# Kernel optimization log

Hardware: AMD Instinct MI355X
Metric: run time of the kernel (lower is better)

Reference implementation:

```python
import jax, jax.numpy as jnp
import numpy as np

N, E, D_IN, D_H, D_OUT = 50000, 800000, 128, 128, 40
EPS = 1e-5


def setup_inputs() -> dict:
    key = jax.random.key(0)
    ks = jax.random.split(key, 12)
    x = jax.random.normal(ks[0], (N, D_IN), dtype=jnp.float32)
    edge_index = jax.random.randint(ks[1], (2, E), 0, N, dtype=jnp.int32)
    s = 1.0 / np.sqrt(D_H)
    return {
        "x": x,
        "edge_index": edge_index,
        "W1": jax.random.normal(ks[2], (D_IN, D_H), jnp.float32) * s,
        "b1": jnp.zeros((D_H,), jnp.float32),
        "W2": jax.random.normal(ks[3], (D_H, D_H), jnp.float32) * s,
        "b2": jnp.zeros((D_H,), jnp.float32),
        "g1": jnp.ones((D_H,), jnp.float32),
        "be1": jnp.zeros((D_H,), jnp.float32),
        "g2": jnp.ones((D_H,), jnp.float32),
        "be2": jnp.zeros((D_H,), jnp.float32),
        "g3": jnp.ones((D_H,), jnp.float32),
        "be3": jnp.zeros((D_H,), jnp.float32),
        "Wm": jax.random.normal(ks[4], (D_H, D_OUT), jnp.float32) * s,
        "bm": jnp.zeros((D_OUT,), jnp.float32),
    }


def _gcn_conv(x, W, b, src, dst, dinv):
    # GCNConv: x' = D^{-1/2}(A+I)D^{-1/2} (x W) + b
    xw = x @ W                                   # [N, H]
    coef = dinv[src] * dinv[dst]                 # [E]
    agg = jax.ops.segment_sum(xw[src] * coef[:, None], dst, num_segments=x.shape[0])
    agg = agg + xw * (dinv * dinv)[:, None]      # self-loop term
    return agg + b


def _bn(x, g, b):
    # BatchNorm1d in training mode: biased batch statistics over nodes
    m = jnp.mean(x, axis=0)
    v = jnp.var(x, axis=0)
    return g * (x - m) * jax.lax.rsqrt(v + EPS) + b


def reference(x, edge_index, W1, b1, W2, b2, g1, be1, g2, be2, g3, be3, Wm, bm):
    src, dst = edge_index[0], edge_index[1]
    # degree with self-loops (GCN symmetric normalization, computed on dst/col)
    deg = 1.0 + jax.ops.segment_sum(jnp.ones((E,), jnp.float32), dst, num_segments=N)
    dinv = jax.lax.rsqrt(deg)
    h = _gcn_conv(x, W1, b1, src, dst, dinv)
    h = jax.nn.relu(_bn(h, g1, be1))            # dropout is identity in eval
    h = _gcn_conv(h, W2, b2, src, dst, dinv)
    h = jax.nn.relu(_bn(h, g2, be2))
    h = _bn(h, g3, be3)
    h = h @ Wm + bm
    return jax.nn.log_softmax(h, axis=1)
```

## Files before the change

### kernel.cpp

```cpp
#include <hip/hip_runtime.h>
#include <hip/hip_fp16.h>
#include <math.h>

#define BN_EPS 1e-5f
#define CAP 128

typedef __attribute__((ext_vector_type(8))) short short8;
typedef __attribute__((ext_vector_type(4))) float floatx4;

__device__ inline unsigned short f2bf(float f) {
    union { float f; unsigned u; } x; x.f = f;
    unsigned r = x.u + 0x7fff + ((x.u >> 16) & 1);
    return (unsigned short)(r >> 16);
}
__device__ inline float bf2f(unsigned short h) {
    union { float f; unsigned u; } x; x.u = ((unsigned)h) << 16; return x.f;
}

__device__ inline void bn_sc_sh(float sum, float sumsq, float g, float be, float invN,
                                float& sc, float& sh) {
    float mean = sum * invN;
    float var = sumsq * invN - mean * mean;
    sc = g * rsqrtf(var + BN_EPS);
    sh = be - mean * sc;
}

__global__ void k_fill_direct(const int* __restrict__ src, const int* __restrict__ dst, int E,
                              int* __restrict__ fillc, unsigned short* __restrict__ col16) {
    int e = blockIdx.x * blockDim.x + threadIdx.x;
    if (e < E) {
        int d = dst[e];
        int r = atomicAdd(&fillc[d], 1);
        if (r < CAP) col16[(size_t)d * CAP + r] = (unsigned short)src[e];
    }
}

__global__ void k_dinv(const int* __restrict__ fillc, float* __restrict__ dinv, int N) {
    int i = blockIdx.x * blockDim.x + threadIdx.x;
    if (i < N) dinv[i] = rsqrtf(1.0f + (float)fillc[i]);
}

__global__ void k_pack_all(const float* __restrict__ W1, const float* __restrict__ W2,
                           const float* __restrict__ Wm, unsigned short* __restrict__ p1,
                           unsigned short* __restrict__ p2, unsigned short* __restrict__ pm) {
    int idx = blockIdx.x * blockDim.x + threadIdx.x;
    const float* W;
    unsigned short* pack;
    int f, l = idx & 63, t, n, stride, ncols;
    if (idx < 2048) {
        W = W1; pack = p1; f = idx >> 6; t = f >> 3; n = (f & 7) * 16 + (l & 15);
        stride = 128; ncols = 128;
    } else if (idx < 4096) {
        W = W2; pack = p2; f = (idx - 2048) >> 6; t = f >> 3; n = (f & 7) * 16 + (l & 15);
        stride = 128; ncols = 128;
    } else if (idx < 4864) {
        W = Wm; pack = pm; f = (idx - 4096) >> 6; t = f / 3; n = (f % 3) * 16 + (l & 15);
        stride = 40; ncols = 40;
    } else {
        return;
    }
    int q = l >> 4;
    unsigned short* p = pack + f * 1024 + l * 16;
#pragma unroll
    for (int j = 0; j < 8; ++j) {
        int k = t * 32 + q * 8 + j;
        float v = (n < ncols) ? W[k * stride + n] : 0.f;
        unsigned short hi = f2bf(v);
        float lo = v - bf2f(hi);
        p[j] = hi;
        p[8 + j] = f2bf(lo);
    }
}

__device__ inline void load_row8(const float* arow, int kbase, float av[8]) {
    float4 a0 = *(const float4*)(arow + kbase);
    float4 a1 = *(const float4*)(arow + kbase + 4);
    av[0] = a0.x; av[1] = a0.y; av[2] = a0.z; av[3] = a0.w;
    av[4] = a1.x; av[5] = a1.y; av[6] = a1.z; av[7] = a1.w;
}
__device__ inline void load_row8(const __half* arow, int kbase, float av[8]) {
    float4 raw = *(const float4*)(arow + kbase);
    const __half2* h = (const __half2*)&raw;
#pragma unroll
    for (int i = 0; i < 4; ++i) {
        float2 f = __half22float2(h[i]);
        av[2 * i] = f.x;
        av[2 * i + 1] = f.y;
    }
}

template <typename T, bool FUSE_BN>
__global__ __launch_bounds__(256) void k_gemm_mfma(const T* __restrict__ A,
                                                   const unsigned short* __restrict__ packW,
                                                   const float* __restrict__ sums,
                                                   const float* __restrict__ g,
                                                   const float* __restrict__ be, float invN,
                                                   const float* __restrict__ dscale,
                                                   __half* __restrict__ C16, int M) {
    int lane = threadIdx.x & 63;
    int wv = threadIdx.x >> 6;
    int m0 = (blockIdx.x * 4 + wv) * 16;
    if (m0 >= M) return;
    int row = lane & 15, quad = lane >> 4;

    floatx4 acc[8];
#pragma unroll
    for (int nt = 0; nt < 8; ++nt) acc[nt] = (floatx4){0.f, 0.f, 0.f, 0.f};

    const T* arow = A + (size_t)(m0 + row) * 128;
#pragma unroll
    for (int t = 0; t < 4; ++t) {
        int kbase = t * 32 + quad * 8;
        float av[8];
        load_row8(arow, kbase, av);
        if (FUSE_BN) {
#pragma unroll
            for (int j = 0; j < 8; ++j) {
                int c = kbase + j;
                float sc, sh;
                bn_sc_sh(sums[c], sums[128 + c], g[c], be[c], invN, sc, sh);
                av[j] = fmaxf(av[j] * sc + sh, 0.f);
            }
        }
        short8 ah, al;
#pragma unroll
        for (int j = 0; j < 8; ++j) {
            unsigned short hi = f2bf(av[j]);
            ah[j] = (short)hi;
            al[j] = (short)f2bf(av[j] - bf2f(hi));
        }
        const unsigned short* wp = packW + (size_t)(t * 8) * 1024 + lane * 16;
#pragma unroll
        for (int nt = 0; nt < 8; ++nt) {
            short8 wh = *(const short8*)wp;
            short8 wl = *(const short8*)(wp + 8);
            wp += 1024;
            acc[nt] = __builtin_amdgcn_mfma_f32_16x16x32_bf16(ah, wh, acc[nt], 0, 0, 0);
            acc[nt] = __builtin_amdgcn_mfma_f32_16x16x32_bf16(al, wh, acc[nt], 0, 0, 0);
            acc[nt] = __builtin_amdgcn_mfma_f32_16x16x32_bf16(ah, wl, acc[nt], 0, 0, 0);
        }
    }

    float d[4];
#pragma unroll
    for (int r = 0; r < 4; ++r) d[r] = dscale[m0 + quad * 4 + r];
#pragma unroll
    for (int nt = 0; nt < 8; ++nt) {
#pragma unroll
        for (int r = 0; r < 4; ++r) {
            C16[(size_t)(m0 + quad * 4 + r) * 128 + nt * 16 + row] =
                __float2half_rn(acc[nt][r] * d[r]);
        }
    }
}

__global__ __launch_bounds__(256) void k_gather(const __half2* __restrict__ y16,
                                                const int* __restrict__ fillc,
                                                const unsigned short* __restrict__ col16,
                                                const float* __restrict__ dinv,
                                                const float* __restrict__ bias,
                                                __half2* __restrict__ out, int N) {
    int wv = threadIdx.x >> 6;
    int lane = threadIdx.x & 63;
    int n = blockIdx.x * 4 + wv;
    if (n >= N) return;
    float2 acc = __half22float2(y16[(size_t)n * 64 + lane]);
    int deg = min(fillc[n], CAP);
    const unsigned short* cb = col16 + (size_t)n * CAP;
    for (int jb = 0; jb < deg; jb += 64) {
        int cnt = min(64, deg - jb);
        int idx = (lane < cnt) ? (int)cb[jb + lane] : 0;
        int jj = 0;
        for (; jj + 8 <= cnt; jj += 8) {
            int s0 = __shfl(idx, jj + 0, 64);
            int s1 = __shfl(idx, jj + 1, 64);
            int s2 = __shfl(idx, jj + 2, 64);
            int s3 = __shfl(idx, jj + 3, 64);
            int s4 = __shfl(idx, jj + 4, 64);
            int s5 = __shfl(idx, jj + 5, 64);
            int s6 = __shfl(idx, jj + 6, 64);
            int s7 = __shfl(idx, jj + 7, 64);
            float2 r0 = __half22float2(y16[(size_t)s0 * 64 + lane]);
            float2 r1 = __half22float2(y16[(size_t)s1 * 64 + lane]);
            float2 r2 = __half22float2(y16[(size_t)s2 * 64 + lane]);
            float2 r3 = __half22float2(y16[(size_t)s3 * 64 + lane]);
            float2 r4 = __half22float2(y16[(size_t)s4 * 64 + lane]);
            float2 r5 = __half22float2(y16[(size_t)s5 * 64 + lane]);
            float2 r6 = __half22float2(y16[(size_t)s6 * 64 + lane]);
            float2 r7 = __half22float2(y16[(size_t)s7 * 64 + lane]);
            acc.x += ((r0.x + r1.x) + (r2.x + r3.x)) + ((r4.x + r5.x) + (r6.x + r7.x));
            acc.y += ((r0.y + r1.y) + (r2.y + r3.y)) + ((r4.y + r5.y) + (r6.y + r7.y));
        }
        for (; jj < cnt; ++jj) {
            int s = __shfl(idx, jj, 64);
            float2 r = __half22float2(y16[(size_t)s * 64 + lane]);
            acc.x += r.x;
            acc.y += r.y;
        }
    }
    float dn = dinv[n];
    float2 b = *(const float2*)&bias[lane << 1];
    float2 o;
    o.x = dn * acc.x + b.x;
    o.y = dn * acc.y + b.y;
    out[(size_t)n * 64 + lane] = __float22half2_rn(o);
}

template <bool TRANSFORM>
__global__ __launch_bounds__(256) void k_stats(const __half2* __restrict__ h, int N,
                                               const float* __restrict__ sums2,
                                               const float* __restrict__ g2,
                                               const float* __restrict__ be2, float invN,
                                               float* __restrict__ stats) {
    int cp = threadIdx.x & 63;
    int rg = threadIdx.x >> 6;
    int rbeg = blockIdx.x * 256;
    int rend = min(rbeg + 256, N);
    float scx = 1.f, shx = 0.f, scy = 1.f, shy = 0.f;
    if (TRANSFORM) {
        int c = cp * 2;
        bn_sc_sh(sums2[c], sums2[128 + c], g2[c], be2[c], invN, scx, shx);
        bn_sc_sh(sums2[c + 1], sums2[128 + c + 1], g2[c + 1], be2[c + 1], invN, scy, shy);
    }
    float sx = 0.f, sy = 0.f, s2x = 0.f, s2y = 0.f;
    for (int r = rbeg + rg; r < rend; r += 4) {
        float2 v = __half22float2(h[(size_t)r * 64 + cp]);
        if (TRANSFORM) {
            v.x = fmaxf(v.x * scx + shx, 0.f);
            v.y = fmaxf(v.y * scy + shy, 0.f);
        }
        sx += v.x; sy += v.y;
        s2x += v.x * v.x; s2y += v.y * v.y;
    }
    __shared__ float ls[4][256];
    ls[0][threadIdx.x] = sx;
    ls[1][threadIdx.x] = sy;
    ls[2][threadIdx.x] = s2x;
    ls[3][threadIdx.x] = s2y;
    __syncthreads();
    if (threadIdx.x < 64) {
        int t = threadIdx.x;
        float a0 = ls[0][t] + ls[0][t + 64] + ls[0][t + 128] + ls[0][t + 192];
        float a1 = ls[1][t] + ls[1][t + 64] + ls[1][t + 128] + ls[1][t + 192];
        float a2 = ls[2][t] + ls[2][t + 64] + ls[2][t + 128] + ls[2][t + 192];
        float a3 = ls[3][t] + ls[3][t + 64] + ls[3][t + 128] + ls[3][t + 192];
        atomicAdd(&stats[2 * t], a0);
        atomicAdd(&stats[2 * t + 1], a1);
        atomicAdd(&stats[128 + 2 * t], a2);
        atomicAdd(&stats[128 + 2 * t + 1], a3);
    }
}

__global__ __launch_bounds__(256) void k_final(const __half* __restrict__ h,
                                               const float* __restrict__ sums2,
                                               const float* __restrict__ g2,
                                               const float* __restrict__ be2,
                                               const float* __restrict__ sums3,
                                               const float* __restrict__ g3,
                                               const float* __restrict__ be3, float invN,
                                               const unsigned short* __restrict__ packWm,
                                               const float* __restrict__ bm,
                                               float* __restrict__ out, int N) {
    int lane = threadIdx.x & 63;
    int wv = threadIdx.x >> 6;
    int m0 = (blockIdx.x * 4 + wv) * 16;
    if (m0 >= N) return;
    int row = lane & 15, quad = lane >> 4;

    floatx4 acc[3];
#pragma unroll
    for (int nt = 0; nt < 3; ++nt) acc[nt] = (floatx4){0.f, 0.f, 0.f, 0.f};

    const __half* arow = h + (size_t)(m0 + row) * 128;
#pragma unroll
    for (int t = 0; t < 4; ++t) {
        int kbase = t * 32 + quad * 8;
        float av[8];
        load_row8(arow, kbase, av);
#pragma unroll
        for (int j = 0; j < 8; ++j) {
            int c = kbase + j;
            float sc2, sh2, sc3, sh3;
            bn_sc_sh(sums2[c], sums2[128 + c], g2[c], be2[c], invN, sc2, sh2);
            bn_sc_sh(sums3[c], sums3[128 + c], g3[c], be3[c], invN, sc3, sh3);
            av[j] = fmaxf(av[j] * sc2 + sh2, 0.f) * sc3 + sh3;
        }
        short8 ah, al;
#pragma unroll
        for (int j = 0; j < 8; ++j) {
            unsigned short hi = f2bf(av[j]);
            ah[j] = (short)hi;
            al[j] = (short)f2bf(av[j] - bf2f(hi));
        }
        const unsigned short* wp = packWm + (size_t)(t * 3) * 1024 + lane * 16;
#pragma unroll
        for (int nt = 0; nt < 3; ++nt) {
            short8 wh = *(const short8*)wp;
            short8 wl = *(const short8*)(wp + 8);
            wp += 1024;
            acc[nt] = __builtin_amdgcn_mfma_f32_16x16x32_bf16(ah, wh, acc[nt], 0, 0, 0);
            acc[nt] = __builtin_amdgcn_mfma_f32_16x16x32_bf16(al, wh, acc[nt], 0, 0, 0);
            acc[nt] = __builtin_amdgcn_mfma_f32_16x16x32_bf16(ah, wl, acc[nt], 0, 0, 0);
        }
    }

    float bb[3];
#pragma unroll
    for (int nt = 0; nt < 3; ++nt) {
        int col = nt * 16 + row;
        bb[nt] = (col < 40) ? bm[col] : 0.f;
    }
    bool val2 = (row < 8);

#pragma unroll
    for (int r = 0; r < 4; ++r) {
        int m = m0 + quad * 4 + r;
        float v0 = acc[0][r] + bb[0];
        float v1 = acc[1][r] + bb[1];
        float v2 = acc[2][r] + bb[2];
        float mx = fmaxf(v0, v1);
        if (val2) mx = fmaxf(mx, v2);
#pragma unroll
        for (int off = 1; off <= 8; off <<= 1) mx = fmaxf(mx, __shfl_xor(mx, off, 64));
        float s = expf(v0 - mx) + expf(v1 - mx) + (val2 ? expf(v2 - mx) : 0.f);
#pragma unroll
        for (int off = 1; off <= 8; off <<= 1) s += __shfl_xor(s, off, 64);
        float lse = mx + logf(s);
        if (m < N) {
            out[(size_t)m * 40 + row] = v0 - lse;
            out[(size_t)m * 40 + 16 + row] = v1 - lse;
            if (val2) out[(size_t)m * 40 + 32 + row] = v2 - lse;
        }
    }
}

extern "C" void kernel_launch(void* const* d_in, const int* in_sizes, int n_in,
                              void* d_out, int out_size, void* d_ws, size_t ws_size,
                              hipStream_t stream) {
    const float* x   = (const float*)d_in[0];
    const int*   ei  = (const int*)d_in[1];
    const float* W1  = (const float*)d_in[2];
    const float* b1  = (const float*)d_in[3];
    const float* W2  = (const float*)d_in[4];
    const float* b2  = (const float*)d_in[5];
    const float* g1  = (const float*)d_in[6];
    const float* be1 = (const float*)d_in[7];
    const float* g2  = (const float*)d_in[8];
    const float* be2 = (const float*)d_in[9];
    const float* g3  = (const float*)d_in[10];
    const float* be3 = (const float*)d_in[11];
    const float* Wm  = (const float*)d_in[12];
    const float* bm  = (const float*)d_in[13];
    float* out = (float*)d_out;

    int N = in_sizes[0] / 128;
    int E = in_sizes[1] / 2;
    const int* srcs = ei;
    const int* dsts = ei + E;
    float invN = 1.0f / (float)N;

    char* ws = (char*)d_ws;
    size_t off = 0;
    auto alloc = [&](size_t bytes) -> void* {
        void* p = ws + off;
        off += (bytes + 255) & ~(size_t)255;
        return p;
    };
    size_t fill_rounded = (((size_t)N * 4) + 255) & ~(size_t)255;
    int*   fillc   = (int*)alloc((size_t)N * 4);
    float* statsAll= (float*)alloc(3 * 256 * 4);
    float* stats1  = statsAll;
    float* stats2  = statsAll + 256;
    float* stats3  = statsAll + 512;
    unsigned short* col16 = (unsigned short*)alloc((size_t)N * CAP * 2);
    float* dinv    = (float*)alloc((size_t)N * 4);
    unsigned short* packW1 = (unsigned short*)alloc(32768 * 2);
    unsigned short* packW2 = (unsigned short*)alloc(32768 * 2);
    unsigned short* packWm = (unsigned short*)alloc(12288 * 2);
    __half* y16 = (__half*)alloc((size_t)N * 128 * 2);
    __half* h16 = (__half*)alloc((size_t)N * 128 * 2);
    (void)ws_size; (void)n_in; (void)out_size;

    hipMemsetAsync(fillc, 0, fill_rounded + 3 * 256 * 4, stream);

    int eb = (E + 255) / 256;
    int nthb = (N + 255) / 256;
    int gb = (N + 63) / 64;
    int gatherb = (N + 3) / 4;

    k_pack_all<<<19, 256, 0, stream>>>(W1, W2, Wm, packW1, packW2, packWm);
    k_fill_direct<<<eb, 256, 0, stream>>>(srcs, dsts, E, fillc, col16);
    k_dinv<<<nthb, 256, 0, stream>>>(fillc, dinv, N);

    k_gemm_mfma<float, false><<<gb, 256, 0, stream>>>(x, packW1, nullptr, nullptr, nullptr,
                                                      invN, dinv, y16, N);
    k_gather<<<gatherb, 256, 0, stream>>>((const __half2*)y16, fillc, col16, dinv, b1,
                                          (__half2*)h16, N);
    k_stats<false><<<nthb, 256, 0, stream>>>((const __half2*)h16, N, nullptr, nullptr, nullptr,
                                             invN, stats1);

    k_gemm_mfma<__half, true><<<gb, 256, 0, stream>>>(h16, packW2, stats1, g1, be1, invN, dinv,
                                                      y16, N);
    k_gather<<<gatherb, 256, 0, stream>>>((const __half2*)y16, fillc, col16, dinv, b2,
                                          (__half2*)h16, N);
    k_stats<false><<<nthb, 256, 0, stream>>>((const __half2*)h16, N, nullptr, nullptr, nullptr,
                                             invN, stats2);

    k_stats<true><<<nthb, 256, 0, stream>>>((const __half2*)h16, N, stats2, g2, be2, invN,
                                            stats3);
    k_final<<<gb, 256, 0, stream>>>(h16, stats2, g2, be2, stats3, g3, be3, invN, packWm, bm,
                                    out, N);
}
```

Before: 335.3 us.

## Fuse whole GCN pipeline into one cooperative persistent kernel with grid syncs

Replaces the chain of about ten separate kernel launches and the memset with a single cooperative persistent kernel. Each stage (pack, CSR fill, GEMM, gather, BN stats, final) runs as a grid-stride phase separated by grid.sync(). The dinv buffer is dropped and degree scaling is recomputed from the fill counts. This removes launch gaps and inter-kernel drain, but adds grid-barrier cost and caps the grid at occupancy-limited residency. A multi-kernel fallback is kept for when the cooperative launch fails.

```diff
diff --git a/kernel.cpp b/kernel.cpp
--- a/kernel.cpp
+++ b/kernel.cpp
@@ -1,9 +1,13 @@
 #include <hip/hip_runtime.h>
 #include <hip/hip_fp16.h>
+#include <hip/hip_cooperative_groups.h>
 #include <math.h>
+
+namespace cg = cooperative_groups;
 
 #define BN_EPS 1e-5f
 #define CAP 128
+#define NSTAT 200
 
 typedef __attribute__((ext_vector_type(8))) short short8;
 typedef __attribute__((ext_vector_type(4))) float floatx4;
@@ -16,7 +20,6 @@
 __device__ inline float bf2f(unsigned short h) {
     union { float f; unsigned u; } x; x.u = ((unsigned)h) << 16; return x.f;
 }
-
 __device__ inline void bn_sc_sh(float sum, float sumsq, float g, float be, float invN,
                                 float& sc, float& sh) {
     float mean = sum * invN;
@@ -25,25 +28,8 @@
     sh = be - mean * sc;
 }
 
-__global__ void k_fill_direct(const int* __restrict__ src, const int* __restrict__ dst, int E,
-                              int* __restrict__ fillc, unsigned short* __restrict__ col16) {
-    int e = blockIdx.x * blockDim.x + threadIdx.x;
-    if (e < E) {
-        int d = dst[e];
-        int r = atomicAdd(&fillc[d], 1);
-        if (r < CAP) col16[(size_t)d * CAP + r] = (unsigned short)src[e];
-    }
-}
-
-__global__ void k_dinv(const int* __restrict__ fillc, float* __restrict__ dinv, int N) {
-    int i = blockIdx.x * blockDim.x + threadIdx.x;
-    if (i < N) dinv[i] = rsqrtf(1.0f + (float)fillc[i]);
-}
-
-__global__ void k_pack_all(const float* __restrict__ W1, const float* __restrict__ W2,
-                           const float* __restrict__ Wm, unsigned short* __restrict__ p1,
-                           unsigned short* __restrict__ p2, unsigned short* __restrict__ pm) {
-    int idx = blockIdx.x * blockDim.x + threadIdx.x;
+__device__ inline void pack_one(int idx, const float* W1, const float* W2, const float* Wm,
+                                unsigned short* p1, unsigned short* p2, unsigned short* pm) {
     const float* W;
     unsigned short* pack;
     int f, l = idx & 63, t, n, stride, ncols;
@@ -53,22 +39,20 @@
     } else if (idx < 4096) {
         W = W2; pack = p2; f = (idx - 2048) >> 6; t = f >> 3; n = (f & 7) * 16 + (l & 15);
         stride = 128; ncols = 128;
-    } else if (idx < 4864) {
+    } else {
         W = Wm; pack = pm; f = (idx - 4096) >> 6; t = f / 3; n = (f % 3) * 16 + (l & 15);
         stride = 40; ncols = 40;
-    } else {
-        return;
     }
     int q = l >> 4;
-    unsigned short* p = pack + f * 1024 + l * 16;
+    unsigned short* pp = pack + f * 1024 + l * 16;
 #pragma unroll
     for (int j = 0; j < 8; ++j) {
         int k = t * 32 + q * 8 + j;
         float v = (n < ncols) ? W[k * stride + n] : 0.f;
         unsigned short hi = f2bf(v);
         float lo = v - bf2f(hi);
-        p[j] = hi;
-        p[8 + j] = f2bf(lo);
+        pp[j] = hi;
+        pp[8 + j] = f2bf(lo);
     }
 }
 
@@ -90,248 +74,358 @@
 }
 
 template <typename T, bool FUSE_BN>
-__global__ __launch_bounds__(256) void k_gemm_mfma(const T* __restrict__ A,
-                                                   const unsigned short* __restrict__ packW,
-                                                   const float* __restrict__ sums,
-                                                   const float* __restrict__ g,
-                                                   const float* __restrict__ be, float invN,
-                                                   const float* __restrict__ dscale,
-                                                   __half* __restrict__ C16, int M) {
-    int lane = threadIdx.x & 63;
-    int wv = threadIdx.x >> 6;
-    int m0 = (blockIdx.x * 4 + wv) * 16;
-    if (m0 >= M) return;
+__device__ void gemm_phase(const T* __restrict__ A, const unsigned short* __restrict__ packW,
+                           const float* __restrict__ sums, const float* __restrict__ g,
+                           const float* __restrict__ be, float invN,
+                           const int* __restrict__ fillc, __half* __restrict__ C16, int M,
+                           int waveId, int nwaves, int lane) {
     int row = lane & 15, quad = lane >> 4;
-
-    floatx4 acc[8];
-#pragma unroll
-    for (int nt = 0; nt < 8; ++nt) acc[nt] = (floatx4){0.f, 0.f, 0.f, 0.f};
-
-    const T* arow = A + (size_t)(m0 + row) * 128;
-#pragma unroll
-    for (int t = 0; t < 4; ++t) {
-        int kbase = t * 32 + quad * 8;
-        float av[8];
-        load_row8(arow, kbase, av);
-        if (FUSE_BN) {
+    for (int m0 = waveId * 16; m0 < M; m0 += nwaves * 16) {
+        floatx4 acc[8];
+#pragma unroll
+        for (int nt = 0; nt < 8; ++nt) acc[nt] = (floatx4){0.f, 0.f, 0.f, 0.f};
+        int mr = m0 + row;
+        if (mr >= M) mr = M - 1;
+        const T* arow = A + (size_t)mr * 128;
+#pragma unroll
+        for (int t = 0; t < 4; ++t) {
+            int kbase = t * 32 + quad * 8;
+            float av[8];
+            load_row8(arow, kbase, av);
+            if (FUSE_BN) {
+#pragma unroll
+                for (int j = 0; j < 8; ++j) {
+                    int c = kbase + j;
+                    float sc, sh;
+                    bn_sc_sh(sums[c], sums[128 + c], g[c], be[c], invN, sc, sh);
+                    av[j] = fmaxf(av[j] * sc + sh, 0.f);
+                }
+            }
+            short8 ah, al;
+#pragma unroll
+            for (int j = 0; j < 8; ++j) {
+                unsigned short hi = f2bf(av[j]);
+                ah[j] = (short)hi;
+                al[j] = (short)f2bf(av[j] - bf2f(hi));
+            }
+            const unsigned short* wp = packW + (size_t)(t * 8) * 1024 + lane * 16;
+#pragma unroll
+            for (int nt = 0; nt < 8; ++nt) {
+                short8 wh = *(const short8*)wp;
+                short8 wl = *(const short8*)(wp + 8);
+                wp += 1024;
+                acc[nt] = __builtin_amdgcn_mfma_f32_16x16x32_bf16(ah, wh, acc[nt], 0, 0, 0);
+                acc[nt] = __builtin_amdgcn_mfma_f32_16x16x32_bf16(al, wh, acc[nt], 0, 0, 0);
+                acc[nt] = __builtin_amdgcn_mfma_f32_16x16x32_bf16(ah, wl, acc[nt], 0, 0, 0);
+            }
+        }
+        float d[4];
+#pragma unroll
+        for (int r = 0; r < 4; ++r) {
+            int m = m0 + quad * 4 + r;
+            d[r] = (m < M) ? rsqrtf(1.f + (float)fillc[m]) : 0.f;
+        }
+#pragma unroll
+        for (int nt = 0; nt < 8; ++nt) {
+#pragma unroll
+            for (int r = 0; r < 4; ++r) {
+                int m = m0 + quad * 4 + r;
+                if (m < M)
+                    C16[(size_t)m * 128 + nt * 16 + row] = __float2half_rn(acc[nt][r] * d[r]);
+            }
+        }
+    }
+}
+
+__device__ void gather_phase(const __half2* __restrict__ y16, const int* __restrict__ fillc,
+                             const unsigned short* __restrict__ col16,
+                             const float* __restrict__ bias, __half2* __restrict__ out, int N,
+                             int waveId, int nwaves, int lane) {
+    for (int n = waveId; n < N; n += nwaves) {
+        float2 acc = __half22float2(y16[(size_t)n * 64 + lane]);
+        int degraw = fillc[n];
+        int deg = min(degraw, CAP);
+        const unsigned short* cb = col16 + (size_t)n * CAP;
+        for (int jb = 0; jb < deg; jb += 64) {
+            int cnt = min(64, deg - jb);
+            int idx = (lane < cnt) ? (int)cb[jb + lane] : 0;
+            int jj = 0;
+            for (; jj + 8 <= cnt; jj += 8) {
+                int s0 = __shfl(idx, jj + 0, 64);
+                int s1 = __shfl(idx, jj + 1, 64);
+                int s2 = __shfl(idx, jj + 2, 64);
+                int s3 = __shfl(idx, jj + 3, 64);
+                int s4 = __shfl(idx, jj + 4, 64);
+                int s5 = __shfl(idx, jj + 5, 64);
+                int s6 = __shfl(idx, jj + 6, 64);
+                int s7 = __shfl(idx, jj + 7, 64);
+                float2 r0 = __half22float2(y16[(size_t)s0 * 64 + lane]);
+                float2 r1 = __half22float2(y16[(size_t)s1 * 64 + lane]);
+                float2 r2 = __half22float2(y16[(size_t)s2 * 64 + lane]);
+                float2 r3 = __half22float2(y16[(size_t)s3 * 64 + lane]);
+                float2 r4 = __half22float2(y16[(size_t)s4 * 64 + lane]);
+                float2 r5 = __half22float2(y16[(size_t)s5 * 64 + lane]);
+                float2 r6 = __half22float2(y16[(size_t)s6 * 64 + lane]);
+                float2 r7 = __half22float2(y16[(size_t)s7 * 64 + lane]);
+                acc.x += ((r0.x + r1.x) + (r2.x + r3.x)) + ((r4.x + r5.x) + (r6.x + r7.x));
+                acc.y += ((r0.y + r1.y) + (r2.y + r3.y)) + ((r4.y + r5.y) + (r6.y + r7.y));
+            }
+            for (; jj < cnt; ++jj) {
+                int s = __shfl(idx, jj, 64);
+                float2 r = __half22float2(y16[(size_t)s * 64 + lane]);
+                acc.x += r.x;
+                acc.y += r.y;
+            }
+        }
+        float dn = rsqrtf(1.f + (float)degraw);
+        float2 b = *(const float2*)&bias[lane << 1];
+        out[(size_t)n * 64 + lane] =
+            __float22half2_rn(make_float2(dn * acc.x + b.x, dn * acc.y + b.y));
+    }
+}
+
+template <bool TRANSFORM>
+__device__ void stats_phase(const __half2* __restrict__ h, int N,
+                            const float* __restrict__ sums2, const float* __restrict__ g2,
+                            const float* __restrict__ be2, float invN,
+                            float* __restrict__ statsOut, int tid, int bid, float (*ls)[256]) {
+    int cp = tid & 63, rg = tid >> 6;
+    float sx = 0.f, sy = 0.f, s2x = 0.f, s2y = 0.f;
+    if (bid < NSTAT) {
+        float scx = 1.f, shx = 0.f, scy = 1.f, shy = 0.f;
+        if (TRANSFORM) {
+            int c = cp * 2;
+            bn_sc_sh(sums2[c], sums2[128 + c], g2[c], be2[c], invN, scx, shx);
+            bn_sc_sh(sums2[c + 1], sums2[128 + c + 1], g2[c + 1], be2[c + 1], invN, scy, shy);
+        }
+        for (int r = bid * 4 + rg; r < N; r += NSTAT * 4) {
+            float2 v = __half22float2(h[(size_t)r * 64 + cp]);
+            if (TRANSFORM) {
+                v.x = fmaxf(v.x * scx + shx, 0.f);
+                v.y = fmaxf(v.y * scy + shy, 0.f);
+            }
+            sx += v.x; sy += v.y;
+            s2x += v.x * v.x; s2y += v.y * v.y;
+        }
+    }
+    __syncthreads();
+    ls[0][tid] = sx; ls[1][tid] = sy; ls[2][tid] = s2x; ls[3][tid] = s2y;
+    __syncthreads();
+    if (bid < NSTAT && tid < 64) {
+        float a0 = ls[0][tid] + ls[0][tid + 64] + ls[0][tid + 128] + ls[0][tid + 192];
+        float a1 = ls[1][tid] + ls[1][tid + 64] + ls[1][tid + 128] + ls[1][tid + 192];
+        float a2 = ls[2][tid] + ls[2][tid + 64] + ls[2][tid + 128] + ls[2][tid + 192];
+        float a3 = ls[3][tid] + ls[3][tid + 64] + ls[3][tid + 128] + ls[3][tid + 192];
+        atomicAdd(&statsOut[2 * tid], a0);
+        atomicAdd(&statsOut[2 * tid + 1], a1);
+        atomicAdd(&statsOut[128 + 2 * tid], a2);
+        atomicAdd(&statsOut[128 + 2 * tid + 1], a3);
+    }
+    __syncthreads();
+}
+
+__device__ void final_phase(const __half* __restrict__ h, const float* __restrict__ sums2,
+                            const float* __restrict__ g2, const float* __restrict__ be2,
+                            const float* __restrict__ sums3, const float* __restrict__ g3,
+                            const float* __restrict__ be3, float invN,
+                            const unsigned short* __restrict__ packWm,
+                            const float* __restrict__ bm, float* __restrict__ out, int N,
+                            int waveId, int nwaves, int lane) {
+    int row = lane & 15, quad = lane >> 4;
+    int units = (N + 15) >> 4;
+    for (int u = waveId; u < units; u += nwaves) {
+        int m0 = u << 4;
+        floatx4 acc[3];
+#pragma unroll
+        for (int nt = 0; nt < 3; ++nt) acc[nt] = (floatx4){0.f, 0.f, 0.f, 0.f};
+        int mr = m0 + row;
+        if (mr >= N) mr = N - 1;
+        const __half* arow = h + (size_t)mr * 128;
+#pragma unroll
+        for (int t = 0; t < 4; ++t) {
+            int kbase = t * 32 + quad * 8;
+            float av[8];
+            load_row8(arow, kbase, av);
 #pragma unroll
             for (int j = 0; j < 8; ++j) {
                 int c = kbase + j;
-                float sc, sh;
-                bn_sc_sh(sums[c], sums[128 + c], g[c], be[c], invN, sc, sh);
-                av[j] = fmaxf(av[j] * sc + sh, 0.f);
-            }
-        }
-        short8 ah, al;
-#pragma unroll
-        for (int j = 0; j < 8; ++j) {
-            unsigned short hi = f2bf(av[j]);
-            ah[j] = (short)hi;
-            al[j] = (short)f2bf(av[j] - bf2f(hi));
-        }
-        const unsigned short* wp = packW + (size_t)(t * 8) * 1024 + lane * 16;
-#pragma unroll
-        for (int nt = 0; nt < 8; ++nt) {
-            short8 wh = *(const short8*)wp;
-            short8 wl = *(const short8*)(wp + 8);
-            wp += 1024;
-            acc[nt] = __builtin_amdgcn_mfma_f32_16x16x32_bf16(ah, wh, acc[nt], 0, 0, 0);
-            acc[nt] = __builtin_amdgcn_mfma_f32_16x16x32_bf16(al, wh, acc[nt], 0, 0, 0);
-            acc[nt] = __builtin_amdgcn_mfma_f32_16x16x32_bf16(ah, wl, acc[nt], 0, 0, 0);
-        }
-    }
-
-    float d[4];
-#pragma unroll
-    for (int r = 0; r < 4; ++r) d[r] = dscale[m0 + quad * 4 + r];
-#pragma unroll
-    for (int nt = 0; nt < 8; ++nt) {
+                float sc2, sh2, sc3, sh3;
+                bn_sc_sh(sums2[c], sums2[128 + c], g2[c], be2[c], invN, sc2, sh2);
+                bn_sc_sh(sums3[c], sums3[128 + c], g3[c], be3[c], invN, sc3, sh3);
+                av[j] = fmaxf(av[j] * sc2 + sh2, 0.f) * sc3 + sh3;
+            }
+            short8 ah, al;
+#pragma unroll
+            for (int j = 0; j < 8; ++j) {
+                unsigned short hi = f2bf(av[j]);
+                ah[j] = (short)hi;
+                al[j] = (short)f2bf(av[j] - bf2f(hi));
+            }
+            const unsigned short* wp = packWm + (size_t)(t * 3) * 1024 + lane * 16;
+#pragma unroll
+            for (int nt = 0; nt < 3; ++nt) {
+                short8 wh = *(const short8*)wp;
+                short8 wl = *(const short8*)(wp + 8);
+                wp += 1024;
+                acc[nt] = __builtin_amdgcn_mfma_f32_16x16x32_bf16(ah, wh, acc[nt], 0, 0, 0);
+                acc[nt] = __builtin_amdgcn_mfma_f32_16x16x32_bf16(al, wh, acc[nt], 0, 0, 0);
+                acc[nt] = __builtin_amdgcn_mfma_f32_16x16x32_bf16(ah, wl, acc[nt], 0, 0, 0);
+            }
+        }
+        float bb[3];
+#pragma unroll
+        for (int nt = 0; nt < 3; ++nt) {
+            int col = nt * 16 + row;
+            bb[nt] = (col < 40) ? bm[col] : 0.f;
+        }
+        bool val2 = (row < 8);
 #pragma unroll
         for (int r = 0; r < 4; ++r) {
-            C16[(size_t)(m0 + quad * 4 + r) * 128 + nt * 16 + row] =
-                __float2half_rn(acc[nt][r] * d[r]);
-        }
-    }
-}
-
-__global__ __launch_bounds__(256) void k_gather(const __half2* __restrict__ y16,
-                                                const int* __restrict__ fillc,
-                                                const unsigned short* __restrict__ col16,
-                                                const float* __restrict__ dinv,
-                                                const float* __restrict__ bias,
-                                                __half2* __restrict__ out, int N) {
-    int wv = threadIdx.x >> 6;
-    int lane = threadIdx.x & 63;
-    int n = blockIdx.x * 4 + wv;
-    if (n >= N) return;
-    float2 acc = __half22float2(y16[(size_t)n * 64 + lane]);
-    int deg = min(fillc[n], CAP);
-    const unsigned short* cb = col16 + (size_t)n * CAP;
-    for (int jb = 0; jb < deg; jb += 64) {
-        int cnt = min(64, deg - jb);
-        int idx = (lane < cnt) ? (int)cb[jb + lane] : 0;
-        int jj = 0;
-        for (; jj + 8 <= cnt; jj += 8) {
-            int s0 = __shfl(idx, jj + 0, 64);
-            int s1 = __shfl(idx, jj + 1, 64);
-            int s2 = __shfl(idx, jj + 2, 64);
-            int s3 = __shfl(idx, jj + 3, 64);
-            int s4 = __shfl(idx, jj + 4, 64);
-            int s5 = __shfl(idx, jj + 5, 64);
-            int s6 = __shfl(idx, jj + 6, 64);
-            int s7 = __shfl(idx, jj + 7, 64);
-            float2 r0 = __half22float2(y16[(size_t)s0 * 64 + lane]);
-            float2 r1 = __half22float2(y16[(size_t)s1 * 64 + lane]);
-            float2 r2 = __half22float2(y16[(size_t)s2 * 64 + lane]);
-            float2 r3 = __half22float2(y16[(size_t)s3 * 64 + lane]);
-            float2 r4 = __half22float2(y16[(size_t)s4 * 64 + lane]);
-            float2 r5 = __half22float2(y16[(size_t)s5 * 64 + lane]);
-            float2 r6 = __half22float2(y16[(size_t)s6 * 64 + lane]);
-            float2 r7 = __half22float2(y16[(size_t)s7 * 64 + lane]);
-            acc.x += ((r0.x + r1.x) + (r2.x + r3.x)) + ((r4.x + r5.x) + (r6.x + r7.x));
-            acc.y += ((r0.y + r1.y) + (r2.y + r3.y)) + ((r4.y + r5.y) + (r6.y + r7.y));
-        }
-        for (; jj < cnt; ++jj) {
-            int s = __shfl(idx, jj, 64);
-            float2 r = __half22float2(y16[(size_t)s * 64 + lane]);
-            acc.x += r.x;
-            acc.y += r.y;
-        }
-    }
-    float dn = dinv[n];
-    float2 b = *(const float2*)&bias[lane << 1];
-    float2 o;
-    o.x = dn * acc.x + b.x;
-    o.y = dn * acc.y + b.y;
-    out[(size_t)n * 64 + lane] = __float22half2_rn(o);
-}
-
-template <bool TRANSFORM>
-__global__ __launch_bounds__(256) void k_stats(const __half2* __restrict__ h, int N,
-                                               const float* __restrict__ sums2,
-                                               const float* __restrict__ g2,
-                                               const float* __restrict__ be2, float invN,
-                                               float* __restrict__ stats) {
-    int cp = threadIdx.x & 63;
-    int rg = threadIdx.x >> 6;
-    int rbeg = blockIdx.x * 256;
-    int rend = min(rbeg + 256, N);
-    float scx = 1.f, shx = 0.f, scy = 1.f, shy = 0.f;
-    if (TRANSFORM) {
-        int c = cp * 2;
-        bn_sc_sh(sums2[c], sums2[128 + c], g2[c], be2[c], invN, scx, shx);
-        bn_sc_sh(sums2[c + 1], sums2[128 + c + 1], g2[c + 1], be2[c + 1], invN, scy, shy);
-    }
-    float sx = 0.f, sy = 0.f, s2x = 0.f, s2y = 0.f;
-    for (int r = rbeg + rg; r < rend; r += 4) {
-        float2 v = __half22float2(h[(size_t)r * 64 + cp]);
-        if (TRANSFORM) {
-            v.x = fmaxf(v.x * scx + shx, 0.f);
-            v.y = fmaxf(v.y * scy + shy, 0.f);
-        }
-        sx += v.x; sy += v.y;
-        s2x += v.x * v.x; s2y += v.y * v.y;
-    }
+            int m = m0 + quad * 4 + r;
+            float v0 = acc[0][r] + bb[0];
+            float v1 = acc[1][r] + bb[1];
+            float v2 = acc[2][r] + bb[2];
+            float mx = fmaxf(v0, v1);
+            if (val2) mx = fmaxf(mx, v2);
+#pragma unroll
+            for (int off = 1; off <= 8; off <<= 1) mx = fmaxf(mx, __shfl_xor(mx, off, 64));
+            float s = expf(v0 - mx) + expf(v1 - mx) + (val2 ? expf(v2 - mx) : 0.f);
+#pragma unroll
+            for (int off = 1; off <= 8; off <<= 1) s += __shfl_xor(s, off, 64);
+            float lse = mx + logf(s);
+            if (m < N) {
+                out[(size_t)m * 40 + row] = v0 - lse;
+                out[(size_t)m * 40 + 16 + row] = v1 - lse;
+                if (val2) out[(size_t)m * 40 + 32 + row] = v2 - lse;
+            }
+        }
+    }
+}
+
+struct MegaParams {
+    const float* x; const int* ei;
+    const float* W1; const float* b1; const float* W2; const float* b2;
+    const float* g1; const float* be1; const float* g2; const float* be2;
+    const float* g3; const float* be3; const float* Wm; const float* bm;
+    int* fillc; float* stats; unsigned short* col16;
+    unsigned short* pW1; unsigned short* pW2; unsigned short* pWm;
+    __half* y16; __half* h16; float* out;
+    int E; int N; float invN;
+};
+
+__global__ void __launch_bounds__(256) k_mega(MegaParams p) {
+    cg::grid_group grid = cg::this_grid();
+    int tid = threadIdx.x, bid = blockIdx.x;
+    int gsz = gridDim.x * 256, gtid = bid * 256 + tid;
+    int lane = tid & 63;
+    int waveId = bid * 4 + (tid >> 6);
+    int nwaves = gridDim.x * 4;
+    const int* srcs = p.ei;
+    const int* dsts = p.ei + p.E;
     __shared__ float ls[4][256];
-    ls[0][threadIdx.x] = sx;
-    ls[1][threadIdx.x] = sy;
-    ls[2][threadIdx.x] = s2x;
-    ls[3][threadIdx.x] = s2y;
-    __syncthreads();
-    if (threadIdx.x < 64) {
-        int t = threadIdx.x;
-        float a0 = ls[0][t] + ls[0][t + 64] + ls[0][t + 128] + ls[0][t + 192];
-        float a1 = ls[1][t] + ls[1][t + 64] + ls[1][t + 128] + ls[1][t + 192];
-        float a2 = ls[2][t] + ls[2][t + 64] + ls[2][t + 128] + ls[2][t + 192];
-        float a3 = ls[3][t] + ls[3][t + 64] + ls[3][t + 128] + ls[3][t + 192];
-        atomicAdd(&stats[2 * t], a0);
-        atomicAdd(&stats[2 * t + 1], a1);
-        atomicAdd(&stats[128 + 2 * t], a2);
-        atomicAdd(&stats[128 + 2 * t + 1], a3);
-    }
-}
-
-__global__ __launch_bounds__(256) void k_final(const __half* __restrict__ h,
-                                               const float* __restrict__ sums2,
-                                               const float* __restrict__ g2,
-                                               const float* __restrict__ be2,
-                                               const float* __restrict__ sums3,
-                                               const float* __restrict__ g3,
-                                               const float* __restrict__ be3, float invN,
-                                               const unsigned short* __restrict__ packWm,
-                                               const float* __restrict__ bm,
-                                               float* __restrict__ out, int N) {
-    int lane = threadIdx.x & 63;
-    int wv = threadIdx.x >> 6;
-    int m0 = (blockIdx.x * 4 + wv) * 16;
-    if (m0 >= N) return;
-    int row = lane & 15, quad = lane >> 4;
-
-    floatx4 acc[3];
-#pragma unroll
-    for (int nt = 0; nt < 3; ++nt) acc[nt] = (floatx4){0.f, 0.f, 0.f, 0.f};
-
-    const __half* arow = h + (size_t)(m0 + row) * 128;
-#pragma unroll
-    for (int t = 0; t < 4; ++t) {
-        int kbase = t * 32 + quad * 8;
-        float av[8];
-        load_row8(arow, kbase, av);
-#pragma unroll
-        for (int j = 0; j < 8; ++j) {
-            int c = kbase + j;
-            float sc2, sh2, sc3, sh3;
-            bn_sc_sh(sums2[c], sums2[128 + c], g2[c], be2[c], invN, sc2, sh2);
-            bn_sc_sh(sums3[c], sums3[128 + c], g3[c], be3[c], invN, sc3, sh3);
-            av[j] = fmaxf(av[j] * sc2 + sh2, 0.f) * sc3 + sh3;
-        }
-        short8 ah, al;
-#pragma unroll
-        for (int j = 0; j < 8; ++j) {
-            unsigned short hi = f2bf(av[j]);
-            ah[j] = (short)hi;
-            al[j] = (short)f2bf(av[j] - bf2f(hi));
-        }
-        const unsigned short* wp = packWm + (size_t)(t * 3) * 1024 + lane * 16;
-#pragma unroll
-        for (int nt = 0; nt < 3; ++nt) {
-            short8 wh = *(const short8*)wp;
-            short8 wl = *(const short8*)(wp + 8);
-            wp += 1024;
-            acc[nt] = __builtin_amdgcn_mfma_f32_16x16x32_bf16(ah, wh, acc[nt], 0, 0, 0);
-            acc[nt] = __builtin_amdgcn_mfma_f32_16x16x32_bf16(al, wh, acc[nt], 0, 0, 0);
-            acc[nt] = __builtin_amdgcn_mfma_f32_16x16x32_bf16(ah, wl, acc[nt], 0, 0, 0);
-        }
-    }
-
-    float bb[3];
-#pragma unroll
-    for (int nt = 0; nt < 3; ++nt) {
-        int col = nt * 16 + row;
-        bb[nt] = (col < 40) ? bm[col] : 0.f;
-    }
-    bool val2 = (row < 8);
-
-#pragma unroll
-    for (int r = 0; r < 4; ++r) {
-        int m = m0 + quad * 4 + r;
-        float v0 = acc[0][r] + bb[0];
-        float v1 = acc[1][r] + bb[1];
-        float v2 = acc[2][r] + bb[2];
-        float mx = fmaxf(v0, v1);
-        if (val2) mx = fmaxf(mx, v2);
-#pragma unroll
-        for (int off = 1; off <= 8; off <<= 1) mx = fmaxf(mx, __shfl_xor(mx, off, 64));
-        float s = expf(v0 - mx) + expf(v1 - mx) + (val2 ? expf(v2 - mx) : 0.f);
-#pragma unroll
-        for (int off = 1; off <= 8; off <<= 1) s += __shfl_xor(s, off, 64);
-        float lse = mx + logf(s);
-        if (m < N) {
-            out[(size_t)m * 40 + row] = v0 - lse;
-            out[(size_t)m * 40 + 16 + row] = v1 - lse;
-            if (val2) out[(size_t)m * 40 + 32 + row] = v2 - lse;
-        }
-    }
+
+    for (int i = gtid; i < p.N; i += gsz) p.fillc[i] = 0;
+    for (int i = gtid; i < 768; i += gsz) p.stats[i] = 0.f;
+    for (int i = gtid; i < 4864; i += gsz) pack_one(i, p.W1, p.W2, p.Wm, p.pW1, p.pW2, p.pWm);
+    __threadfence();
+    grid.sync();
+
+    for (int e = gtid; e < p.E; e += gsz) {
+        int d = dsts[e];
+        int r = atomicAdd(&p.fillc[d], 1);
+        if (r < CAP) p.col16[(size_t)d * CAP + r] = (unsigned short)srcs[e];
+    }
+    __threadfence();
+    grid.sync();
+
+    gemm_phase<float, false>(p.x, p.pW1, nullptr, nullptr, nullptr, p.invN, p.fillc, p.y16,
+                             p.N, waveId, nwaves, lane);
+    __threadfence();
+    grid.sync();
+
+    gather_phase((const __half2*)p.y16, p.fillc, p.col16, p.b1, (__half2*)p.h16, p.N, waveId,
+                 nwaves, lane);
+    __threadfence();
+    grid.sync();
+
+    stats_phase<false>((const __half2*)p.h16, p.N, nullptr, nullptr, nullptr, p.invN, p.stats,
+                       tid, bid, ls);
+    __threadfence();
+    grid.sync();
+
+    gemm_phase<__half, true>(p.h16, p.pW2, p.stats, p.g1, p.be1, p.invN, p.fillc, p.y16, p.N,
+                             waveId, nwaves, lane);
+    __threadfence();
+    grid.sync();
+
+    gather_phase((const __half2*)p.y16, p.fillc, p.col16, p.b2, (__half2*)p.h16, p.N, waveId,
+                 nwaves, lane);
+    __threadfence();
+    grid.sync();
+
+    stats_phase<false>((const __half2*)p.h16, p.N, nullptr, nullptr, nullptr, p.invN,
+                       p.stats + 256, tid, bid, ls);
+    __threadfence();
+    grid.sync();
+
+    stats_phase<true>((const __half2*)p.h16, p.N, p.stats + 256, p.g2, p.be2, p.invN,
+                      p.stats + 512, tid, bid, ls);
+    __threadfence();
+    grid.sync();
+
+    final_phase(p.h16, p.stats + 256, p.g2, p.be2, p.stats + 512, p.g3, p.be3, p.invN, p.pWm,
+                p.bm, p.out, p.N, waveId, nwaves, lane);
+}
+
+__global__ void k_pack(const float* W1, const float* W2, const float* Wm, unsigned short* p1,
+                       unsigned short* p2, unsigned short* pm) {
+    int idx = blockIdx.x * blockDim.x + threadIdx.x;
+    if (idx < 4864) pack_one(idx, W1, W2, Wm, p1, p2, pm);
+}
+__global__ void k_fill(const int* src, const int* dst, int E, int* fillc,
+                       unsigned short* col16) {
+    int e = blockIdx.x * blockDim.x + threadIdx.x;
+    if (e < E) {
+        int d = dst[e];
+        int r = atomicAdd(&fillc[d], 1);
+        if (r < CAP) col16[(size_t)d * CAP + r] = (unsigned short)src[e];
+    }
+}
+__global__ __launch_bounds__(256) void k_gemm1(const float* A, const unsigned short* pW,
+                                               const int* fillc, __half* C, int M) {
+    gemm_phase<float, false>(A, pW, nullptr, nullptr, nullptr, 0.f, fillc, C, M,
+                             blockIdx.x * 4 + (threadIdx.x >> 6), gridDim.x * 4,
+                             threadIdx.x & 63);
+}
+__global__ __launch_bounds__(256) void k_gemm2(const __half* A, const unsigned short* pW,
+                                               const float* sums, const float* g,
+                                               const float* be, float invN, const int* fillc,
+                                               __half* C, int M) {
+    gemm_phase<__half, true>(A, pW, sums, g, be, invN, fillc, C, M,
+                             blockIdx.x * 4 + (threadIdx.x >> 6), gridDim.x * 4,
+                             threadIdx.x & 63);
+}
+__global__ __launch_bounds__(256) void k_gath(const __half2* y, const int* fillc,
+                                              const unsigned short* col16, const float* bias,
+                                              __half2* out, int N) {
+    gather_phase(y, fillc, col16, bias, out, N, blockIdx.x * 4 + (threadIdx.x >> 6),
+                 gridDim.x * 4, threadIdx.x & 63);
+}
+template <bool TR>
+__global__ __launch_bounds__(256) void k_stats_s(const __half2* h, int N, const float* sums2,
+                                                 const float* g2, const float* be2, float invN,
+                                                 float* statsOut) {
+    __shared__ float ls[4][256];
+    stats_phase<TR>(h, N, sums2, g2, be2, invN, statsOut, threadIdx.x, blockIdx.x, ls);
+}
+__global__ __launch_bounds__(256) void k_final_s(const __half* h, const float* sums2,
+                                                 const float* g2, const float* be2,
+                                                 const float* sums3, const float* g3,
+                                                 const float* be3, float invN,
+                                                 const unsigned short* pWm, const float* bm,
+                                                 float* out, int N) {
+    final_phase(h, sums2, g2, be2, sums3, g3, be3, invN, pWm, bm, out, N,
+                blockIdx.x * 4 + (threadIdx.x >> 6), gridDim.x * 4, threadIdx.x & 63);
 }
 
 extern "C" void kernel_launch(void* const* d_in, const int* in_sizes, int n_in,
@@ -355,8 +449,6 @@
 
     int N = in_sizes[0] / 128;
     int E = in_sizes[1] / 2;
-    const int* srcs = ei;
-    const int* dsts = ei + E;
     float invN = 1.0f / (float)N;
 
     char* ws = (char*)d_ws;
@@ -367,47 +459,55 @@
         return p;
     };
     size_t fill_rounded = (((size_t)N * 4) + 255) & ~(size_t)255;
-    int*   fillc   = (int*)alloc((size_t)N * 4);
-    float* statsAll= (float*)alloc(3 * 256 * 4);
-    float* stats1  = statsAll;
-    float* stats2  = statsAll + 256;
-    float* stats3  = statsAll + 512;
+    int*   fillc    = (int*)alloc((size_t)N * 4);
+    float* statsAll = (float*)alloc(768 * 4);
     unsigned short* col16 = (unsigned short*)alloc((size_t)N * CAP * 2);
-    float* dinv    = (float*)alloc((size_t)N * 4);
-    unsigned short* packW1 = (unsigned short*)alloc(32768 * 2);
-    unsigned short* packW2 = (unsigned short*)alloc(32768 * 2);
-    unsigned short* packWm = (unsigned short*)alloc(12288 * 2);
+    unsigned short* pW1 = (unsigned short*)alloc(32768 * 2);
+    unsigned short* pW2 = (unsigned short*)alloc(32768 * 2);
+    unsigned short* pWm = (unsigned short*)alloc(12288 * 2);
     __half* y16 = (__half*)alloc((size_t)N * 128 * 2);
     __half* h16 = (__half*)alloc((size_t)N * 128 * 2);
     (void)ws_size; (void)n_in; (void)out_size;
 
-    hipMemsetAsync(fillc, 0, fill_rounded + 3 * 256 * 4, stream);
-
-    int eb = (E + 255) / 256;
-    int nthb = (N + 255) / 256;
-    int gb = (N + 63) / 64;
-    int gatherb = (N + 3) / 4;
-
-    k_pack_all<<<19, 256, 0, stream>>>(W1, W2, Wm, packW1, packW2, packWm);
-    k_fill_direct<<<eb, 256, 0, stream>>>(srcs, dsts, E, fillc, col16);
-    k_dinv<<<nthb, 256, 0, stream>>>(fillc, dinv, N);
-
-    k_gemm_mfma<float, false><<<gb, 256, 0, stream>>>(x, packW1, nullptr, nullptr, nullptr,
-                                                      invN, dinv, y16, N);
-    k_gather<<<gatherb, 256, 0, stream>>>((const __half2*)y16, fillc, col16, dinv, b1,
-                                          (__half2*)h16, N);
-    k_stats<false><<<nthb, 256, 0, stream>>>((const __half2*)h16, N, nullptr, nullptr, nullptr,
-                                             invN, stats1);
-
-    k_gemm_mfma<__half, true><<<gb, 256, 0, stream>>>(h16, packW2, stats1, g1, be1, invN, dinv,
-                                                      y16, N);
-    k_gather<<<gatherb, 256, 0, stream>>>((const __half2*)y16, fillc, col16, dinv, b2,
-                                          (__half2*)h16, N);
-    k_stats<false><<<nthb, 256, 0, stream>>>((const __half2*)h16, N, nullptr, nullptr, nullptr,
-                                             invN, stats2);
-
-    k_stats<true><<<nthb, 256, 0, stream>>>((const __half2*)h16, N, stats2, g2, be2, invN,
-                                            stats3);
-    k_final<<<gb, 256, 0, stream>>>(h16, stats2, g2, be2, stats3, g3, be3, invN, packWm, bm,
-                                    out, N);
-}
+    MegaParams p;
+    p.x = x; p.ei = ei; p.W1 = W1; p.b1 = b1; p.W2 = W2; p.b2 = b2;
+    p.g1 = g1; p.be1 = be1; p.g2 = g2; p.be2 = be2; p.g3 = g3; p.be3 = be3;
+    p.Wm = Wm; p.bm = bm;
+    p.fillc = fillc; p.stats = statsAll; p.col16 = col16;
+    p.pW1 = pW1; p.pW2 = pW2; p.pWm = pWm;
+    p.y16 = y16; p.h16 = h16; p.out = out;
+    p.E = E; p.N = N; p.invN = invN;
+
+    int maxb = 0;
+    hipError_t qerr = hipOccupancyMaxActiveBlocksPerMultiprocessor(&maxb, k_mega, 256, 0);
+    if (qerr != hipSuccess || maxb < 1) maxb = 1;
+    if (maxb > 8) maxb = 8;
+    int grid = maxb * 256;
+
+    void* args[] = {&p};
+    hipError_t lerr =
+        hipLaunchCooperativeKernel((void*)k_mega, dim3(grid), dim3(256), args, 0, stream);
+
+    if (lerr != hipSuccess) {
+        hipMemsetAsync(fillc, 0, fill_rounded + 768 * 4, stream);
+        int eb = (E + 255) / 256;
+        int gb = (N + 63) / 64;
+        int gatherb = (N + 3) / 4;
+        k_pack<<<19, 256, 0, stream>>>(W1, W2, Wm, pW1, pW2, pWm);
+        k_fill<<<eb, 256, 0, stream>>>(ei, ei + E, E, fillc, col16);
+        k_gemm1<<<gb, 256, 0, stream>>>(x, pW1, fillc, y16, N);
+        k_gath<<<gatherb, 256, 0, stream>>>((const __half2*)y16, fillc, col16, b1,
+                                            (__half2*)h16, N);
+        k_stats_s<false><<<NSTAT, 256, 0, stream>>>((const __half2*)h16, N, nullptr, nullptr,
+                                                    nullptr, invN, statsAll);
+        k_gemm2<<<gb, 256, 0, stream>>>(h16, pW2, statsAll, g1, be1, invN, fillc, y16, N);
+        k_gath<<<gatherb, 256, 0, stream>>>((const __half2*)y16, fillc, col16, b2,
+                                            (__half2*)h16, N);
+        k_stats_s<false><<<NSTAT, 256, 0, stream>>>((const __half2*)h16, N, nullptr, nullptr,
+                                                    nullptr, invN, statsAll + 256);
+        k_stats_s<true><<<NSTAT, 256, 0, stream>>>((const __half2*)h16, N, statsAll + 256, g2,
+                                                   be2, invN, statsAll + 512);
+        k_final_s<<<gb, 256, 0, stream>>>(h16, statsAll + 256, g2, be2, statsAll + 512, g3,
+                                          be3, invN, pWm, bm, out, N);
+    }
+}
```

After: 1.007 ms. +200.4%, slower.
